# Kernel tuning notes

Hardware: AMD Instinct MI355X
Metric: run time of the kernel (lower is better)

The kernel has to match this reference:

```python
import jax, jax.numpy as jnp
import numpy as np

N_NODES = 50000
N_EDGES = 500000
HID = 128
NLAYERS = 4
NGRAPHS = 64
NODE_F = 15
EDGE_F = 3


def _init(key, shape, fan_in):
    return jax.random.normal(key, shape, dtype=jnp.float32) / np.sqrt(fan_in)


def setup_inputs() -> dict:
    key = jax.random.key(0)
    ks = jax.random.split(key, 32)
    inp = {}
    inp["x"] = jax.random.normal(ks[0], (N_NODES, NODE_F), dtype=jnp.float32)
    inp["edge_index"] = jax.random.randint(ks[1], (2, N_EDGES), 0, N_NODES, dtype=jnp.int64)
    inp["edge_attr"] = jax.random.normal(ks[2], (N_EDGES, EDGE_F), dtype=jnp.float32)
    inp["pos"] = jax.random.normal(ks[3], (N_NODES, 3), dtype=jnp.float32)
    inp["batch"] = jnp.sort(jax.random.randint(ks[4], (N_NODES,), 0, NGRAPHS, dtype=jnp.int64))
    # encoders
    inp["enc_w"] = _init(ks[5], (NODE_F, HID), NODE_F)
    inp["enc_b"] = jnp.zeros((HID,), jnp.float32)
    inp["eenc_w"] = _init(ks[6], (EDGE_F, HID), EDGE_F)
    inp["eenc_b"] = jnp.zeros((HID,), jnp.float32)
    # stacked per-layer conv params
    MIN = 2 * HID + 1  # message input dim = 257
    inp["msg_w1"] = _init(ks[7], (NLAYERS, MIN, HID), MIN)
    inp["msg_b1"] = jnp.zeros((NLAYERS, HID), jnp.float32)
    inp["msg_w2"] = _init(ks[8], (NLAYERS, HID, HID), HID)
    inp["msg_b2"] = jnp.zeros((NLAYERS, HID), jnp.float32)
    inp["upd_w1"] = _init(ks[9], (NLAYERS, 2 * HID, HID), 2 * HID)
    inp["upd_b1"] = jnp.zeros((NLAYERS, HID), jnp.float32)
    inp["upd_w2"] = _init(ks[10], (NLAYERS, HID, HID), HID)
    inp["upd_b2"] = jnp.zeros((NLAYERS, HID), jnp.float32)
    inp["ln_g"] = jnp.ones((NLAYERS, HID), jnp.float32)
    inp["ln_b"] = jnp.zeros((NLAYERS, HID), jnp.float32)
    # readout MLP (dropout is eval-mode identity)
    inp["mlp_w1"] = _init(ks[11], (HID, HID), HID)
    inp["mlp_b1"] = jnp.zeros((HID,), jnp.float32)
    inp["mlp_w2"] = _init(ks[12], (HID, HID // 2), HID)
    inp["mlp_b2"] = jnp.zeros((HID // 2,), jnp.float32)
    inp["mlp_w3"] = _init(ks[13], (HID // 2, 1), HID // 2)
    inp["mlp_b3"] = jnp.zeros((1,), jnp.float32)
    return inp


def reference(x, edge_index, edge_attr, pos, batch,
              enc_w, enc_b, eenc_w, eenc_b,
              msg_w1, msg_b1, msg_w2, msg_b2,
              upd_w1, upd_b1, upd_w2, upd_b2,
              ln_g, ln_b,
              mlp_w1, mlp_b1, mlp_w2, mlp_b2, mlp_w3, mlp_b3):
    n = x.shape[0]
    h = x @ enc_w + enc_b                      # [N, H] node encoder
    _ea = edge_attr @ eenc_w + eenc_b          # encoded but unused downstream (faithful to source)
    src = edge_index[0]                        # j (source)
    dst = edge_index[1]                        # i (target)
    dist = jnp.linalg.norm(pos[dst] - pos[src], axis=-1, keepdims=True)  # [E,1]
    for i in range(NLAYERS):
        xi = h[dst]
        xj = h[src]
        m_in = jnp.concatenate([xi, xj, dist], axis=-1)               # [E, 2H+1]
        m = jax.nn.relu(m_in @ msg_w1[i] + msg_b1[i]) @ msg_w2[i] + msg_b2[i]
        aggr = jax.ops.segment_sum(m, dst, num_segments=n)            # scatter-add -> [N,H]
        u_in = jnp.concatenate([h, aggr], axis=-1)                    # [N, 2H]
        u = jax.nn.relu(u_in @ upd_w1[i] + upd_b1[i]) @ upd_w2[i] + upd_b2[i]
        mu = jnp.mean(u, axis=-1, keepdims=True)
        var = jnp.mean((u - mu) ** 2, axis=-1, keepdims=True)
        u = (u - mu) / jnp.sqrt(var + 1e-5) * ln_g[i] + ln_b[i]
        u = jax.nn.relu(u)
        h = u if i == 0 else h + u
    # global mean pool over graphs
    cnt = jax.ops.segment_sum(jnp.ones((n, 1), h.dtype), batch, num_segments=NGRAPHS)
    pooled = jax.ops.segment_sum(h, batch, num_segments=NGRAPHS) / jnp.maximum(cnt, 1.0)
    o = jax.nn.relu(pooled @ mlp_w1 + mlp_b1)
    o = jax.nn.relu(o @ mlp_w2 + mlp_b2)
    return o @ mlp_w3 + mlp_b3                  # [NGRAPHS, 1]
```

## Files before the change

### kernel.cpp

```cpp
#include <hip/hip_runtime.h>
#include <hip/hip_bf16.h>
#include <cstdint>

#define N_NODES 50000
#define N_EDGES 500000
#define HID 128
#define NLAYERS 4
#define NGRAPHS 64
#define NTILES ((N_NODES + 63) / 64)
#define NPW 4
#define EBLOCKS ((N_NODES + NPW * 4 - 1) / (NPW * 4))

typedef float f32x4 __attribute__((ext_vector_type(4)));
typedef __bf16 bf16x8 __attribute__((ext_vector_type(8)));

__device__ float          g_h[(size_t)N_NODES * HID];
__device__ unsigned short g_hb[(size_t)N_NODES * HID];
__device__ float          g_S[(size_t)N_NODES * HID];
__device__ unsigned short g_PQ[(size_t)N_NODES * 256];
__device__ float          g_dists[N_EDGES];
__device__ int            g_srcs[N_EDGES];
__device__ int            g_cnt[N_NODES];
__device__ int            g_cursor[N_NODES];
__device__ int            g_bsum[1024];
__device__ unsigned short g_pqw[NLAYERS * 4 * 16 * 64 * 8];
__device__ float          g_wc[NLAYERS * 128 * 128];
__device__ float          g_bc[NLAYERS * 128];
__device__ unsigned short g_uw1p[NLAYERS * 8 * 8 * 64 * 8];
__device__ unsigned short g_uw2p[NLAYERS * 4 * 8 * 64 * 8];
__device__ float          g_pooled[NGRAPHS * HID];

__device__ __forceinline__ unsigned short f2bf(float f) {
    uint32_t u = __builtin_bit_cast(uint32_t, f);
    uint32_t r = (u + 0x7fffu + ((u >> 16) & 1u)) >> 16;
    return (unsigned short)r;
}
__device__ __forceinline__ float bf2f(unsigned short u) {
    return __builtin_bit_cast(float, (uint32_t)u << 16);
}

__global__ void clear_cnt_k() {
    int i = blockIdx.x * 256 + threadIdx.x;
    if (i < N_NODES) g_cnt[i] = 0;
}
__global__ void clear_pooled_k() {
    int i = blockIdx.x * 256 + threadIdx.x;
    if (i < NGRAPHS * HID) g_pooled[i] = 0.f;
}

__global__ void pack_pqw_k(const float* __restrict__ w1) {
    int lane = threadIdx.x;
    int bid = blockIdx.x;
    int nt = bid & 15, ks = (bid >> 4) & 3, L = bid >> 6;
    const float* w = w1 + (size_t)L * 257 * HID;
    int kb = ks * 32 + (lane >> 4) * 8;
    int n = nt * 16 + (lane & 15);
    unsigned short tmp[8];
#pragma unroll
    for (int j = 0; j < 8; ++j) {
        int k = kb + j;
        float v = (n < 128) ? w[(size_t)k * HID + n] : w[(size_t)(128 + k) * HID + (n - 128)];
        tmp[j] = f2bf(v);
    }
    uint4 o = make_uint4(tmp[0] | ((uint32_t)tmp[1] << 16), tmp[2] | ((uint32_t)tmp[3] << 16),
                         tmp[4] | ((uint32_t)tmp[5] << 16), tmp[6] | ((uint32_t)tmp[7] << 16));
    *(uint4*)&g_pqw[(((size_t)(L * 4 + ks) * 16 + nt) * 64 + lane) * 8] = o;
}

__global__ void wc_k(const float* __restrict__ mw2, const float* __restrict__ uw1) {
    __shared__ float row[128];
    int L = blockIdx.x >> 7, k = blockIdx.x & 127, j = threadIdx.x;
    row[j] = mw2[(size_t)L * 128 * 128 + k * 128 + j];
    __syncthreads();
    const float* u1b = uw1 + (size_t)L * 256 * 128 + 128 * 128;
    float s = 0.f;
    for (int i = 0; i < 128; ++i) s += row[i] * u1b[i * 128 + j];
    g_wc[(size_t)L * 128 * 128 + k * 128 + j] = s;
}
__global__ void bc_k(const float* __restrict__ mb2, const float* __restrict__ uw1) {
    int L = blockIdx.x, j = threadIdx.x;
    const float* u1b = uw1 + (size_t)L * 256 * 128 + 128 * 128;
    const float* b2 = mb2 + L * 128;
    float s = 0.f;
    for (int i = 0; i < 128; ++i) s += b2[i] * u1b[i * 128 + j];
    g_bc[L * 128 + j] = s;
}

__global__ void pack_u1_k(const float* __restrict__ uw1) {
    int lane = threadIdx.x;
    int bid = blockIdx.x;
    int nt = bid & 7, ks = (bid >> 3) & 7, L = bid >> 6;
    int kb = ks * 32 + (lane >> 4) * 8;
    int n = nt * 16 + (lane & 15);
    unsigned short tmp[8];
#pragma unroll
    for (int j = 0; j < 8; ++j) {
        int k = kb + j;
        float v = (k < 128) ? uw1[(size_t)L * 256 * 128 + (size_t)k * 128 + n]
                            : g_wc[(size_t)L * 128 * 128 + (size_t)(k - 128) * 128 + n];
        tmp[j] = f2bf(v);
    }
    uint4 o = make_uint4(tmp[0] | ((uint32_t)tmp[1] << 16), tmp[2] | ((uint32_t)tmp[3] << 16),
                         tmp[4] | ((uint32_t)tmp[5] << 16), tmp[6] | ((uint32_t)tmp[7] << 16));
    *(uint4*)&g_uw1p[(((size_t)(L * 8 + ks) * 8 + nt) * 64 + lane) * 8] = o;
}

__global__ void pack_w2_k(const float* __restrict__ uw2) {
    int lane = threadIdx.x;
    int bid = blockIdx.x;
    int nt = bid & 7, ks = (bid >> 3) & 3, L = bid >> 5;
    int kb = ks * 32 + (lane >> 4) * 8;
    int n = nt * 16 + (lane & 15);
    unsigned short tmp[8];
#pragma unroll
    for (int j = 0; j < 8; ++j)
        tmp[j] = f2bf(uw2[(size_t)L * 128 * 128 + (size_t)(kb + j) * 128 + n]);
    uint4 o = make_uint4(tmp[0] | ((uint32_t)tmp[1] << 16), tmp[2] | ((uint32_t)tmp[3] << 16),
                         tmp[4] | ((uint32_t)tmp[5] << 16), tmp[6] | ((uint32_t)tmp[7] << 16));
    *(uint4*)&g_uw2p[(((size_t)(L * 4 + ks) * 8 + nt) * 64 + lane) * 8] = o;
}

__global__ void encode_k(const float* __restrict__ x, const float* __restrict__ w,
                         const float* __restrict__ b) {
    __shared__ float xl[2][15];
    int t = threadIdx.x;
    int half = t >> 7;
    int node = blockIdx.x * 2 + half;
    int c = t & 127;
    if (c < 15) xl[half][c] = x[(size_t)node * 15 + c];
    __syncthreads();
    float acc = b[c];
#pragma unroll
    for (int k = 0; k < 15; ++k) acc += xl[half][k] * w[k * HID + c];
    g_h[(size_t)node * HID + c] = acc;
    g_hb[(size_t)node * HID + c] = f2bf(acc);
}

__global__ void hist_k(const int* __restrict__ ei) {
    int e = blockIdx.x * 256 + threadIdx.x;
    if (e < N_EDGES) atomicAdd(&g_cnt[ei[N_EDGES + e]], 1);
}
__global__ void scanA_k() {
    __shared__ int s[512];
    int t = threadIdx.x;
    int i = blockIdx.x * 512 + t;
    s[t] = (i < N_NODES) ? g_cnt[i] : 0;
    __syncthreads();
    for (int d = 256; d > 0; d >>= 1) {
        if (t < d) s[t] += s[t + d];
        __syncthreads();
    }
    if (t == 0) g_bsum[blockIdx.x] = s[0];
}
__global__ void scanB_k(int nb) {
    if (threadIdx.x == 0) {
        int acc = 0;
        for (int i = 0; i < nb; ++i) { int v = g_bsum[i]; g_bsum[i] = acc; acc += v; }
    }
}
__global__ void scanC_k() {
    __shared__ int s[512];
    int t = threadIdx.x;
    int i = blockIdx.x * 512 + t;
    int v = (i < N_NODES) ? g_cnt[i] : 0;
    s[t] = v;
    __syncthreads();
    for (int d = 1; d < 512; d <<= 1) {
        int add = (t >= d) ? s[t - d] : 0;
        __syncthreads();
        s[t] += add;
        __syncthreads();
    }
    if (i < N_NODES) g_cursor[i] = g_bsum[blockIdx.x] + s[t] - v;
}
__global__ void scatter_k(const int* __restrict__ ei, const float* __restrict__ pos) {
    int e = blockIdx.x * 256 + threadIdx.x;
    if (e >= N_EDGES) return;
    int s = ei[e];
    int d = ei[N_EDGES + e];
    float dx = pos[d * 3 + 0] - pos[s * 3 + 0];
    float dy = pos[d * 3 + 1] - pos[s * 3 + 1];
    float dz = pos[d * 3 + 2] - pos[s * 3 + 2];
    int p = atomicAdd(&g_cursor[d], 1);
    g_srcs[p] = s;
    g_dists[p] = sqrtf(dx * dx + dy * dy + dz * dz);
}

__global__ __launch_bounds__(256, 2)
void pq_k(int L) {
    __shared__ unsigned short Abuf[64 * 128];
    __shared__ unsigned short Obuf[64 * 264];
    const unsigned short* wp = g_pqw + (size_t)L * 4 * 16 * 64 * 8;
    int t = threadIdx.x, wave = t >> 6, lane = t & 63;
    int arow = lane & 15, kgrp = lane >> 4;
    int tile0 = blockIdx.x * 64;

    {
        int r = t >> 2, p = t & 3;
        int n = tile0 + r;
        bool valid = n < N_NODES;
#pragma unroll
        for (int q = 0; q < 4; ++q) {
            int slot = p * 4 + q;
            uint4 v = make_uint4(0, 0, 0, 0);
            if (valid) v = *(const uint4*)&g_hb[(size_t)n * HID + slot * 8];
            *(uint4*)&Abuf[r * 128 + ((slot ^ (r & 7)) << 3)] = v;
        }
    }
    __syncthreads();

    bf16x8 wv[4][4];
#pragma unroll
    for (int ks = 0; ks < 4; ++ks)
#pragma unroll
        for (int ntl = 0; ntl < 4; ++ntl)
            wv[ks][ntl] = *(const bf16x8*)&wp[((size_t)(ks * 16 + wave * 4 + ntl) * 64 + lane) * 8];

    f32x4 acc[4][4];
#pragma unroll
    for (int rf = 0; rf < 4; ++rf)
#pragma unroll
        for (int ntl = 0; ntl < 4; ++ntl) acc[rf][ntl] = (f32x4){0.f, 0.f, 0.f, 0.f};
#pragma unroll
    for (int ks = 0; ks < 4; ++ks) {
        int slot = ks * 4 + kgrp;
#pragma unroll
        for (int rf = 0; rf < 4; ++rf) {
            int row = rf * 16 + arow;
            bf16x8 a = *(const bf16x8*)&Abuf[row * 128 + ((slot ^ (row & 7)) << 3)];
#pragma unroll
            for (int ntl = 0; ntl < 4; ++ntl)
                acc[rf][ntl] = __builtin_amdgcn_mfma_f32_16x16x32_bf16(a, wv[ks][ntl], acc[rf][ntl], 0, 0, 0);
        }
    }
#pragma unroll
    for (int rf = 0; rf < 4; ++rf)
#pragma unroll
        for (int ntl = 0; ntl < 4; ++ntl) {
            int col = wave * 64 + ntl * 16 + arow;
#pragma unroll
            for (int q = 0; q < 4; ++q) {
                int row = rf * 16 + kgrp * 4 + q;
                Obuf[row * 264 + col] = f2bf(acc[rf][ntl][q]);
            }
        }
    __syncthreads();
#pragma unroll
    for (int i = 0; i < 8; ++i) {
        int k = t + i * 256;
        int row = k >> 5, cc = k & 31;
        int n = tile0 + row;
        if (n < N_NODES)
            *(uint4*)&g_PQ[(size_t)n * 256 + cc * 8] = *(const uint4*)&Obuf[row * 264 + cc * 8];
    }
}

__global__ __launch_bounds__(256, 8)
void edge_relu_k(const float* __restrict__ w1last, const float* __restrict__ b1) {
    int t = threadIdx.x, wave = t >> 6, lane = t & 63;
    int c2 = lane * 2;
    float wl0 = w1last[c2], wl1 = w1last[c2 + 1];
    float bb0 = b1[c2], bb1 = b1[c2 + 1];

    int gw = blockIdx.x * 4 + wave;
    int n0 = gw * NPW;
    int n1 = n0 + NPW < N_NODES ? n0 + NPW : N_NODES;

    for (int n = n0; n < n1; ++n) {
        int end = g_cursor[n];
        int cnt = g_cnt[n];
        int beg = end - cnt;
        uint32_t pv = *(const uint32_t*)&g_PQ[(size_t)n * 256 + c2];
        float pb0 = bf2f((unsigned short)(pv & 0xffff)) + bb0;
        float pb1 = bf2f((unsigned short)(pv >> 16)) + bb1;
        float acc0 = 0.f, acc1 = 0.f;

        for (int cb = beg; cb < end; cb += 64) {
            int mye = cb + lane;
            bool v = mye < end;
            int msrc = v ? g_srcs[mye] : 0;
            float mdist = v ? g_dists[mye] : 0.f;
            int lim = end - cb < 64 ? end - cb : 64;
            int full = lim & ~7;
            for (int b = 0; b < full; b += 8) {
                uint32_t qv[8];
#pragma unroll
                for (int j = 0; j < 8; ++j) {
                    int s = __shfl(msrc, b + j);
                    qv[j] = *(const uint32_t*)&g_PQ[(size_t)s * 256 + 128 + c2];
                }
#pragma unroll
                for (int j = 0; j < 8; ++j) {
                    float dist = __shfl(mdist, b + j);
                    acc0 += fmaxf(fmaf(dist, wl0, pb0 + bf2f((unsigned short)(qv[j] & 0xffff))), 0.f);
                    acc1 += fmaxf(fmaf(dist, wl1, pb1 + bf2f((unsigned short)(qv[j] >> 16))), 0.f);
                }
            }
            for (int j = full; j < lim; ++j) {
                int s = __shfl(msrc, j);
                float dist = __shfl(mdist, j);
                uint32_t qv = *(const uint32_t*)&g_PQ[(size_t)s * 256 + 128 + c2];
                acc0 += fmaxf(fmaf(dist, wl0, pb0 + bf2f((unsigned short)(qv & 0xffff))), 0.f);
                acc1 += fmaxf(fmaf(dist, wl1, pb1 + bf2f((unsigned short)(qv >> 16))), 0.f);
            }
        }
        *(float2*)&g_S[(size_t)n * HID + c2] = make_float2(acc0, acc1);
    }
}

__global__ __launch_bounds__(256, 4)
void upd_k(const float* __restrict__ ub1, const float* __restrict__ ub2,
           const float* __restrict__ lng, const float* __restrict__ lnb,
           int L, int first_layer, int Lpq) {
    __shared__ unsigned short Abuf[64 * 128];
    __shared__ unsigned short Hbuf[64 * 128];
    __shared__ float rsums[2][2][64];
    __shared__ float degb[64];
    const unsigned short* w1p = g_uw1p + (size_t)L * 8 * 8 * 64 * 8;
    const unsigned short* w2p = g_uw2p + (size_t)L * 4 * 8 * 64 * 8;
    int t = threadIdx.x, wave = t >> 6, lane = t & 63;
    int wr = wave >> 1, wc = wave & 1;
    int arow = lane & 15, kgrp = lane >> 4;
    int tile0 = blockIdx.x * 64;

    int sr = t >> 2, sp = t & 3;
    int sn = tile0 + sr;
    bool svalid = sn < N_NODES;

    if (sp == 0) degb[sr] = svalid ? (float)g_cnt[sn] : 0.f;
#pragma unroll
    for (int q = 0; q < 4; ++q) {
        int slot = sp * 4 + q;
        uint4 v = make_uint4(0, 0, 0, 0);
        if (svalid) v = *(const uint4*)&g_hb[(size_t)sn * HID + slot * 8];
        *(uint4*)&Abuf[sr * 128 + ((slot ^ (sr & 7)) << 3)] = v;
    }
    __syncthreads();

    f32x4 acc0[4], acc1[4];
#pragma unroll
    for (int i = 0; i < 4; ++i) { acc0[i] = (f32x4){0.f,0.f,0.f,0.f}; acc1[i] = (f32x4){0.f,0.f,0.f,0.f}; }
    int r0 = wr * 32 + arow, r1 = r0 + 16;
#pragma unroll
    for (int ks = 0; ks < 4; ++ks) {
        int slot = ks * 4 + kgrp;
        bf16x8 a0 = *(const bf16x8*)&Abuf[r0 * 128 + ((slot ^ (arow & 7)) << 3)];
        bf16x8 a1 = *(const bf16x8*)&Abuf[r1 * 128 + ((slot ^ (arow & 7)) << 3)];
#pragma unroll
        for (int ntl = 0; ntl < 4; ++ntl) {
            bf16x8 b = *(const bf16x8*)&w1p[((size_t)(ks * 8 + wc * 4 + ntl) * 64 + lane) * 8];
            acc0[ntl] = __builtin_amdgcn_mfma_f32_16x16x32_bf16(a0, b, acc0[ntl], 0, 0, 0);
            acc1[ntl] = __builtin_amdgcn_mfma_f32_16x16x32_bf16(a1, b, acc1[ntl], 0, 0, 0);
        }
    }
    __syncthreads();

#pragma unroll
    for (int q = 0; q < 4; ++q) {
        int slot = sp * 4 + q;
        uint4 v = make_uint4(0, 0, 0, 0);
        if (svalid) {
            const float* spt = &g_S[(size_t)sn * HID + slot * 8];
            float4 f0 = *(const float4*)spt;
            float4 f1 = *((const float4*)spt + 1);
            v.x = f2bf(f0.x) | ((uint32_t)f2bf(f0.y) << 16);
            v.y = f2bf(f0.z) | ((uint32_t)f2bf(f0.w) << 16);
            v.z = f2bf(f1.x) | ((uint32_t)f2bf(f1.y) << 16);
            v.w = f2bf(f1.z) | ((uint32_t)f2bf(f1.w) << 16);
        }
        *(uint4*)&Abuf[sr * 128 + ((slot ^ (sr & 7)) << 3)] = v;
    }
    __syncthreads();

#pragma unroll
    for (int ks = 0; ks < 4; ++ks) {
        int slot = ks * 4 + kgrp;
        bf16x8 a0 = *(const bf16x8*)&Abuf[r0 * 128 + ((slot ^ (arow & 7)) << 3)];
        bf16x8 a1 = *(const bf16x8*)&Abuf[r1 * 128 + ((slot ^ (arow & 7)) << 3)];
#pragma unroll
        for (int ntl = 0; ntl < 4; ++ntl) {
            bf16x8 b = *(const bf16x8*)&w1p[((size_t)((ks + 4) * 8 + wc * 4 + ntl) * 64 + lane) * 8];
            acc0[ntl] = __builtin_amdgcn_mfma_f32_16x16x32_bf16(a0, b, acc0[ntl], 0, 0, 0);
            acc1[ntl] = __builtin_amdgcn_mfma_f32_16x16x32_bf16(a1, b, acc1[ntl], 0, 0, 0);
        }
    }

    float dg0[4], dg1[4];
#pragma unroll
    for (int q = 0; q < 4; ++q) {
        dg0[q] = degb[wr * 32 + kgrp * 4 + q];
        dg1[q] = degb[wr * 32 + 16 + kgrp * 4 + q];
    }
#pragma unroll
    for (int ntl = 0; ntl < 4; ++ntl) {
        int col = wc * 64 + ntl * 16 + arow;
        float bv1 = ub1[col], bcv = g_bc[L * 128 + col];
        int slotH = col >> 3, cl = col & 7;
#pragma unroll
        for (int q = 0; q < 4; ++q) {
            int rw0 = wr * 32 + kgrp * 4 + q;
            float h0 = fmaxf(acc0[ntl][q] + dg0[q] * bcv + bv1, 0.f);
            Hbuf[rw0 * 128 + ((slotH ^ (rw0 & 7)) << 3) + cl] = f2bf(h0);
            int rw1 = rw0 + 16;
            float h1 = fmaxf(acc1[ntl][q] + dg1[q] * bcv + bv1, 0.f);
            Hbuf[rw1 * 128 + ((slotH ^ (rw1 & 7)) << 3) + cl] = f2bf(h1);
        }
    }
    __syncthreads();

    f32x4 c0[4], c1[4];
#pragma unroll
    for (int i = 0; i < 4; ++i) { c0[i] = (f32x4){0.f,0.f,0.f,0.f}; c1[i] = (f32x4){0.f,0.f,0.f,0.f}; }
#pragma unroll
    for (int ks = 0; ks < 4; ++ks) {
        int slot = ks * 4 + kgrp;
        bf16x8 a0 = *(const bf16x8*)&Hbuf[r0 * 128 + ((slot ^ (arow & 7)) << 3)];
        bf16x8 a1 = *(const bf16x8*)&Hbuf[r1 * 128 + ((slot ^ (arow & 7)) << 3)];
#pragma unroll
        for (int ntl = 0; ntl < 4; ++ntl) {
            bf16x8 b = *(const bf16x8*)&w2p[((size_t)(ks * 8 + wc * 4 + ntl) * 64 + lane) * 8];
            c0[ntl] = __builtin_amdgcn_mfma_f32_16x16x32_bf16(a0, b, c0[ntl], 0, 0, 0);
            c1[ntl] = __builtin_amdgcn_mfma_f32_16x16x32_bf16(a1, b, c1[ntl], 0, 0, 0);
        }
    }

    float bv2[4], gm[4], bt[4];
#pragma unroll
    for (int ntl = 0; ntl < 4; ++ntl) {
        int col = wc * 64 + ntl * 16 + arow;
        bv2[ntl] = ub2[col]; gm[ntl] = lng[col]; bt[ntl] = lnb[col];
    }
    float s0[4] = {0,0,0,0}, s1[4] = {0,0,0,0}, q0[4] = {0,0,0,0}, q1[4] = {0,0,0,0};
#pragma unroll
    for (int ntl = 0; ntl < 4; ++ntl)
#pragma unroll
        for (int q = 0; q < 4; ++q) {
            float v0 = c0[ntl][q] + bv2[ntl];
            float v1 = c1[ntl][q] + bv2[ntl];
            c0[ntl][q] = v0; c1[ntl][q] = v1;
            s0[q] += v0; q0[q] += v0 * v0;
            s1[q] += v1; q1[q] += v1 * v1;
        }
#pragma unroll
    for (int m = 1; m < 16; m <<= 1)
#pragma unroll
        for (int q = 0; q < 4; ++q) {
            s0[q] += __shfl_xor(s0[q], m); q0[q] += __shfl_xor(q0[q], m);
            s1[q] += __shfl_xor(s1[q], m); q1[q] += __shfl_xor(q1[q], m);
        }
    if (arow == 0) {
#pragma unroll
        for (int q = 0; q < 4; ++q) {
            int rw0 = wr * 32 + kgrp * 4 + q;
            rsums[wc][0][rw0] = s0[q]; rsums[wc][1][rw0] = q0[q];
            rsums[wc][0][rw0 + 16] = s1[q]; rsums[wc][1][rw0 + 16] = q1[q];
        }
    }
    __syncthreads();

    float mean0[4], rstd0[4], mean1[4], rstd1[4];
#pragma unroll
    for (int q = 0; q < 4; ++q) {
        int rw0 = wr * 32 + kgrp * 4 + q;
        float sm = rsums[0][0][rw0] + rsums[1][0][rw0];
        float sq = rsums[0][1][rw0] + rsums[1][1][rw0];
        mean0[q] = sm * (1.f / HID);
        rstd0[q] = rsqrtf(sq * (1.f / HID) - mean0[q] * mean0[q] + 1e-5f);
        int rw1 = rw0 + 16;
        sm = rsums[0][0][rw1] + rsums[1][0][rw1];
        sq = rsums[0][1][rw1] + rsums[1][1][rw1];
        mean1[q] = sm * (1.f / HID);
        rstd1[q] = rsqrtf(sq * (1.f / HID) - mean1[q] * mean1[q] + 1e-5f);
    }

#pragma unroll
    for (int ntl = 0; ntl < 4; ++ntl) {
        int col = wc * 64 + ntl * 16 + arow;
        int slotA = col >> 3, clA = col & 7;
#pragma unroll
        for (int q = 0; q < 4; ++q) {
            int rw0 = wr * 32 + kgrp * 4 + q;
            int row0 = tile0 + rw0;
            float u0 = fmaxf((c0[ntl][q] - mean0[q]) * rstd0[q] * gm[ntl] + bt[ntl], 0.f);
            float hr0 = (!first_layer && row0 < N_NODES) ? g_h[(size_t)row0 * HID + col] : 0.f;
            float hn0 = first_layer ? u0 : (hr0 + u0);
            c0[ntl][q] = hn0;
            Abuf[rw0 * 128 + ((slotA ^ (rw0 & 7)) << 3) + clA] = f2bf(hn0);
            int rw1 = rw0 + 16;
            int row1 = row0 + 16;
            float u1 = fmaxf((c1[ntl][q] - mean1[q]) * rstd1[q] * gm[ntl] + bt[ntl], 0.f);
            float hr1 = (!first_layer && row1 < N_NODES) ? g_h[(size_t)row1 * HID + col] : 0.f;
            float hn1 = first_layer ? u1 : (hr1 + u1);
            c1[ntl][q] = hn1;
            Abuf[rw1 * 128 + ((slotA ^ (rw1 & 7)) << 3) + clA] = f2bf(hn1);
        }
    }
    __syncthreads();

    float* FB = (float*)Hbuf;
#pragma unroll
    for (int h = 0; h < 2; ++h) {
        if (wr == h) {
#pragma unroll
            for (int ntl = 0; ntl < 4; ++ntl) {
                int col = wc * 64 + ntl * 16 + arow;
#pragma unroll
                for (int q = 0; q < 4; ++q) {
                    int lr = kgrp * 4 + q;
                    FB[lr * 128 + col] = c0[ntl][q];
                    FB[(lr + 16) * 128 + col] = c1[ntl][q];
                }
            }
        }
        __syncthreads();
#pragma unroll
        for (int i = 0; i < 4; ++i) {
            int pos = t + i * 256;
            int row = pos >> 5, cc = pos & 31;
            int n = tile0 + h * 32 + row;
            if (n < N_NODES)
                *(float4*)&g_h[(size_t)n * HID + cc * 4] = *(const float4*)&FB[row * 128 + cc * 4];
        }
        __syncthreads();
    }

    if (Lpq < 0) return;

#pragma unroll
    for (int i = 0; i < 4; ++i) {
        int pos = t + i * 256;
        int row = pos >> 4, s = pos & 15;
        int n = tile0 + row;
        if (n < N_NODES)
            *(uint4*)&g_hb[(size_t)n * HID + s * 8] =
                *(const uint4*)&Abuf[row * 128 + ((s ^ (row & 7)) << 3)];
    }

    const unsigned short* wp = g_pqw + (size_t)Lpq * 4 * 16 * 64 * 8;
#pragma unroll
    for (int h = 0; h < 2; ++h) {
        bf16x8 w3[4][2];
#pragma unroll
        for (int ks = 0; ks < 4; ++ks)
#pragma unroll
            for (int j = 0; j < 2; ++j) {
                int nt = h * 8 + wave * 2 + j;
                w3[ks][j] = *(const bf16x8*)&wp[((size_t)(ks * 16 + nt) * 64 + lane) * 8];
            }
        f32x4 a3[4][2];
#pragma unroll
        for (int rf = 0; rf < 4; ++rf)
#pragma unroll
            for (int j = 0; j < 2; ++j) a3[rf][j] = (f32x4){0.f, 0.f, 0.f, 0.f};
#pragma unroll
        for (int ks = 0; ks < 4; ++ks) {
            int slot = ks * 4 + kgrp;
#pragma unroll
            for (int rf = 0; rf < 4; ++rf) {
                int row = rf * 16 + arow;
                bf16x8 a = *(const bf16x8*)&Abuf[row * 128 + ((slot ^ (arow & 7)) << 3)];
#pragma unroll
                for (int j = 0; j < 2; ++j)
                    a3[rf][j] = __builtin_amdgcn_mfma_f32_16x16x32_bf16(a, w3[ks][j], a3[rf][j], 0, 0, 0);
            }
        }
        __syncthreads();
#pragma unroll
        for (int rf = 0; rf < 4; ++rf)
#pragma unroll
            for (int j = 0; j < 2; ++j) {
                int cl2 = (wave * 2 + j) * 16 + arow;
                int slotP = cl2 >> 3, clP = cl2 & 7;
#pragma unroll
                for (int q = 0; q < 4; ++q) {
                    int row = rf * 16 + kgrp * 4 + q;
                    Hbuf[row * 128 + ((slotP ^ (row & 7)) << 3) + clP] = f2bf(a3[rf][j][q]);
                }
            }
        __syncthreads();
#pragma unroll
        for (int i = 0; i < 4; ++i) {
            int u = t + i * 256;
            int row = u >> 4, s = u & 15;
            int n2 = tile0 + row;
            if (n2 < N_NODES)
                *(uint4*)&g_PQ[(size_t)n2 * 256 + h * 128 + s * 8] =
                    *(const uint4*)&Hbuf[row * 128 + ((s ^ (row & 7)) << 3)];
        }
    }
}

__global__ __launch_bounds__(256, 8)
void pool_k(const int* __restrict__ batch) {
    __shared__ int se[2];
    __shared__ float part[2][128];
    int b = blockIdx.x;
    int g = b >> 3, sub = b & 7;
    int t = threadIdx.x;
    if (t == 0) {
        int lo = 0, hi = N_NODES;
        while (lo < hi) { int m = (lo + hi) >> 1; if (batch[m] < g) lo = m + 1; else hi = m; }
        se[0] = lo;
        hi = N_NODES;
        while (lo < hi) { int m = (lo + hi) >> 1; if (batch[m] < g + 1) lo = m + 1; else hi = m; }
        se[1] = lo;
    }
    __syncthreads();
    int s = se[0], e = se[1];
    int c = t & 127, half = t >> 7;
    float acc = 0.f;
    for (int n = s + sub * 2 + half; n < e; n += 16) acc += g_h[(size_t)n * HID + c];
    part[half][c] = acc;
    __syncthreads();
    if (t < 128) {
        float v = part[0][t] + part[1][t];
        atomicAdd(&g_pooled[g * HID + t], v);
    }
}

__global__ void readout_k(const int* __restrict__ batch,
                          const float* __restrict__ w1, const float* __restrict__ b1,
                          const float* __restrict__ w2, const float* __restrict__ b2,
                          const float* __restrict__ w3, const float* __restrict__ b3,
                          float* __restrict__ out) {
    __shared__ float p[128], o1[128], o2[64];
    __shared__ int se[2];
    int g = blockIdx.x, t = threadIdx.x;
    if (t == 0) {
        int lo = 0, hi = N_NODES;
        while (lo < hi) { int m = (lo + hi) >> 1; if (batch[m] < g) lo = m + 1; else hi = m; }
        se[0] = lo;
        hi = N_NODES;
        while (lo < hi) { int m = (lo + hi) >> 1; if (batch[m] < g + 1) lo = m + 1; else hi = m; }
        se[1] = lo;
    }
    __syncthreads();
    float cntf = fmaxf((float)(se[1] - se[0]), 1.f);
    p[t] = g_pooled[g * HID + t] / cntf;
    __syncthreads();
    float a = b1[t];
    for (int k = 0; k < 128; ++k) a += p[k] * w1[k * 128 + t];
    o1[t] = fmaxf(a, 0.f);
    __syncthreads();
    if (t < 64) {
        float a2 = b2[t];
        for (int k = 0; k < 128; ++k) a2 += o1[k] * w2[k * 64 + t];
        o2[t] = fmaxf(a2, 0.f);
    }
    __syncthreads();
    if (t == 0) {
        float a3 = b3[0];
        for (int k = 0; k < 64; ++k) a3 += o2[k] * w3[k];
        out[g] = a3;
    }
}

extern "C" void kernel_launch(void* const* d_in, const int* in_sizes, int n_in,
                              void* d_out, int out_size, void* d_ws, size_t ws_size,
                              hipStream_t stream) {
    const float* x     = (const float*)d_in[0];
    const int*   ei    = (const int*)d_in[1];
    const float* pos   = (const float*)d_in[3];
    const int*   batch = (const int*)d_in[4];
    const float* enc_w = (const float*)d_in[5];
    const float* enc_b = (const float*)d_in[6];
    const float* msg_w1 = (const float*)d_in[9];
    const float* msg_b1 = (const float*)d_in[10];
    const float* msg_w2 = (const float*)d_in[11];
    const float* msg_b2 = (const float*)d_in[12];
    const float* upd_w1 = (const float*)d_in[13];
    const float* upd_b1 = (const float*)d_in[14];
    const float* upd_w2 = (const float*)d_in[15];
    const float* upd_b2 = (const float*)d_in[16];
    const float* ln_g   = (const float*)d_in[17];
    const float* ln_b   = (const float*)d_in[18];
    const float* mw1 = (const float*)d_in[19];
    const float* mb1 = (const float*)d_in[20];
    const float* mw2 = (const float*)d_in[21];
    const float* mb2 = (const float*)d_in[22];
    const float* mw3 = (const float*)d_in[23];
    const float* mb3 = (const float*)d_in[24];
    float* out = (float*)d_out;
    (void)d_ws; (void)ws_size; (void)in_sizes; (void)n_in; (void)out_size;

    pack_pqw_k<<<NLAYERS * 4 * 16, 64, 0, stream>>>(msg_w1);
    wc_k<<<NLAYERS * 128, 128, 0, stream>>>(msg_w2, upd_w1);
    bc_k<<<NLAYERS, 128, 0, stream>>>(msg_b2, upd_w1);
    pack_u1_k<<<NLAYERS * 8 * 8, 64, 0, stream>>>(upd_w1);
    pack_w2_k<<<NLAYERS * 4 * 8, 64, 0, stream>>>(upd_w2);

    encode_k<<<N_NODES / 2, 256, 0, stream>>>(x, enc_w, enc_b);

    clear_cnt_k<<<(N_NODES + 255) / 256, 256, 0, stream>>>();
    hist_k<<<(N_EDGES + 255) / 256, 256, 0, stream>>>(ei);
    int nb = (N_NODES + 511) / 512;
    scanA_k<<<nb, 512, 0, stream>>>();
    scanB_k<<<1, 64, 0, stream>>>(nb);
    scanC_k<<<nb, 512, 0, stream>>>();
    scatter_k<<<(N_EDGES + 255) / 256, 256, 0, stream>>>(ei, pos);

    pq_k<<<NTILES, 256, 0, stream>>>(0);
    clear_pooled_k<<<32, 256, 0, stream>>>();
    for (int L = 0; L < NLAYERS; ++L) {
        edge_relu_k<<<EBLOCKS, 256, 0, stream>>>(
            msg_w1 + (size_t)L * 257 * HID + 256 * HID, msg_b1 + L * HID);
        upd_k<<<NTILES, 256, 0, stream>>>(
            upd_b1 + L * HID, upd_b2 + L * HID, ln_g + L * HID, ln_b + L * HID,
            L, L == 0 ? 1 : 0, L < NLAYERS - 1 ? L + 1 : -1);
    }

    pool_k<<<NGRAPHS * 8, 256, 0, stream>>>(batch);
    readout_k<<<NGRAPHS, 128, 0, stream>>>(batch, mw1, mb1, mw2, mb2, mw3, mb3, out);
}
```

Baseline: 561.9 us.

## Shrink update-kernel tiles to 32 rows and pack edge src/dist into int2

The update kernel now processes 32-node tiles instead of 64, with each of the four waves owning a 32-column slice and all 32 rows. This halves shared memory per block, raises the occupancy hint from 4 to 6, and launches twice as many blocks. Separately, the CSR edge arrays (source index and distance) are merged into one int2 array so the edge kernel fetches both with a single load. Smaller tiles reload the weights more often per node, and the LayerNorm reduction now sums four partials instead of two.

```diff
diff --git a/kernel.cpp b/kernel.cpp
--- a/kernel.cpp
+++ b/kernel.cpp
@@ -8,6 +8,7 @@
 #define NLAYERS 4
 #define NGRAPHS 64
 #define NTILES ((N_NODES + 63) / 64)
+#define NT32 ((N_NODES + 31) / 32)
 #define NPW 4
 #define EBLOCKS ((N_NODES + NPW * 4 - 1) / (NPW * 4))
 
@@ -18,8 +19,7 @@
 __device__ unsigned short g_hb[(size_t)N_NODES * HID];
 __device__ float          g_S[(size_t)N_NODES * HID];
 __device__ unsigned short g_PQ[(size_t)N_NODES * 256];
-__device__ float          g_dists[N_EDGES];
-__device__ int            g_srcs[N_EDGES];
+__device__ int2           g_edge[N_EDGES];
 __device__ int            g_cnt[N_NODES];
 __device__ int            g_cursor[N_NODES];
 __device__ int            g_bsum[1024];
@@ -181,9 +181,9 @@
     float dx = pos[d * 3 + 0] - pos[s * 3 + 0];
     float dy = pos[d * 3 + 1] - pos[s * 3 + 1];
     float dz = pos[d * 3 + 2] - pos[s * 3 + 2];
+    float dist = sqrtf(dx * dx + dy * dy + dz * dz);
     int p = atomicAdd(&g_cursor[d], 1);
-    g_srcs[p] = s;
-    g_dists[p] = sqrtf(dx * dx + dy * dy + dz * dz);
+    g_edge[p] = make_int2(s, __builtin_bit_cast(int, dist));
 }
 
 __global__ __launch_bounds__(256, 2)
@@ -278,8 +278,9 @@
         for (int cb = beg; cb < end; cb += 64) {
             int mye = cb + lane;
             bool v = mye < end;
-            int msrc = v ? g_srcs[mye] : 0;
-            float mdist = v ? g_dists[mye] : 0.f;
+            int2 ed = v ? g_edge[mye] : make_int2(0, 0);
+            int msrc = ed.x;
+            float mdist = __builtin_bit_cast(float, ed.y);
             int lim = end - cb < 64 ? end - cb : 64;
             int full = lim & ~7;
             for (int b = 0; b < full; b += 8) {
@@ -308,47 +309,46 @@
     }
 }
 
-__global__ __launch_bounds__(256, 4)
+__global__ __launch_bounds__(256, 6)
 void upd_k(const float* __restrict__ ub1, const float* __restrict__ ub2,
            const float* __restrict__ lng, const float* __restrict__ lnb,
            int L, int first_layer, int Lpq) {
-    __shared__ unsigned short Abuf[64 * 128];
-    __shared__ unsigned short Hbuf[64 * 128];
-    __shared__ float rsums[2][2][64];
-    __shared__ float degb[64];
+    __shared__ unsigned short Abuf[32 * 128];
+    __shared__ unsigned short Hbuf[32 * 128];
+    __shared__ float rsums[4][2][32];
+    __shared__ float degb[32];
     const unsigned short* w1p = g_uw1p + (size_t)L * 8 * 8 * 64 * 8;
     const unsigned short* w2p = g_uw2p + (size_t)L * 4 * 8 * 64 * 8;
     int t = threadIdx.x, wave = t >> 6, lane = t & 63;
-    int wr = wave >> 1, wc = wave & 1;
     int arow = lane & 15, kgrp = lane >> 4;
-    int tile0 = blockIdx.x * 64;
-
-    int sr = t >> 2, sp = t & 3;
+    int tile0 = blockIdx.x * 32;
+
+    int sr = t >> 3, sp = t & 7;
     int sn = tile0 + sr;
     bool svalid = sn < N_NODES;
 
     if (sp == 0) degb[sr] = svalid ? (float)g_cnt[sn] : 0.f;
 #pragma unroll
-    for (int q = 0; q < 4; ++q) {
-        int slot = sp * 4 + q;
+    for (int q = 0; q < 2; ++q) {
+        int slot = sp * 2 + q;
         uint4 v = make_uint4(0, 0, 0, 0);
         if (svalid) v = *(const uint4*)&g_hb[(size_t)sn * HID + slot * 8];
         *(uint4*)&Abuf[sr * 128 + ((slot ^ (sr & 7)) << 3)] = v;
     }
     __syncthreads();
 
-    f32x4 acc0[4], acc1[4];
-#pragma unroll
-    for (int i = 0; i < 4; ++i) { acc0[i] = (f32x4){0.f,0.f,0.f,0.f}; acc1[i] = (f32x4){0.f,0.f,0.f,0.f}; }
-    int r0 = wr * 32 + arow, r1 = r0 + 16;
+    f32x4 acc0[2], acc1[2];
+#pragma unroll
+    for (int i = 0; i < 2; ++i) { acc0[i] = (f32x4){0.f,0.f,0.f,0.f}; acc1[i] = (f32x4){0.f,0.f,0.f,0.f}; }
+    int r0 = arow, r1 = arow + 16;
 #pragma unroll
     for (int ks = 0; ks < 4; ++ks) {
         int slot = ks * 4 + kgrp;
         bf16x8 a0 = *(const bf16x8*)&Abuf[r0 * 128 + ((slot ^ (arow & 7)) << 3)];
         bf16x8 a1 = *(const bf16x8*)&Abuf[r1 * 128 + ((slot ^ (arow & 7)) << 3)];
 #pragma unroll
-        for (int ntl = 0; ntl < 4; ++ntl) {
-            bf16x8 b = *(const bf16x8*)&w1p[((size_t)(ks * 8 + wc * 4 + ntl) * 64 + lane) * 8];
+        for (int ntl = 0; ntl < 2; ++ntl) {
+            bf16x8 b = *(const bf16x8*)&w1p[((size_t)(ks * 8 + wave * 2 + ntl) * 64 + lane) * 8];
             acc0[ntl] = __builtin_amdgcn_mfma_f32_16x16x32_bf16(a0, b, acc0[ntl], 0, 0, 0);
             acc1[ntl] = __builtin_amdgcn_mfma_f32_16x16x32_bf16(a1, b, acc1[ntl], 0, 0, 0);
         }
@@ -356,8 +356,8 @@
     __syncthreads();
 
 #pragma unroll
-    for (int q = 0; q < 4; ++q) {
-        int slot = sp * 4 + q;
+    for (int q = 0; q < 2; ++q) {
+        int slot = sp * 2 + q;
         uint4 v = make_uint4(0, 0, 0, 0);
         if (svalid) {
             const float* spt = &g_S[(size_t)sn * HID + slot * 8];
@@ -378,8 +378,8 @@
         bf16x8 a0 = *(const bf16x8*)&Abuf[r0 * 128 + ((slot ^ (arow & 7)) << 3)];
         bf16x8 a1 = *(const bf16x8*)&Abuf[r1 * 128 + ((slot ^ (arow & 7)) << 3)];
 #pragma unroll
-        for (int ntl = 0; ntl < 4; ++ntl) {
-            bf16x8 b = *(const bf16x8*)&w1p[((size_t)((ks + 4) * 8 + wc * 4 + ntl) * 64 + lane) * 8];
+        for (int ntl = 0; ntl < 2; ++ntl) {
+            bf16x8 b = *(const bf16x8*)&w1p[((size_t)((ks + 4) * 8 + wave * 2 + ntl) * 64 + lane) * 8];
             acc0[ntl] = __builtin_amdgcn_mfma_f32_16x16x32_bf16(a0, b, acc0[ntl], 0, 0, 0);
             acc1[ntl] = __builtin_amdgcn_mfma_f32_16x16x32_bf16(a1, b, acc1[ntl], 0, 0, 0);
         }
@@ -388,17 +388,17 @@
     float dg0[4], dg1[4];
 #pragma unroll
     for (int q = 0; q < 4; ++q) {
-        dg0[q] = degb[wr * 32 + kgrp * 4 + q];
-        dg1[q] = degb[wr * 32 + 16 + kgrp * 4 + q];
-    }
-#pragma unroll
-    for (int ntl = 0; ntl < 4; ++ntl) {
-        int col = wc * 64 + ntl * 16 + arow;
+        dg0[q] = degb[kgrp * 4 + q];
+        dg1[q] = degb[16 + kgrp * 4 + q];
+    }
+#pragma unroll
+    for (int ntl = 0; ntl < 2; ++ntl) {
+        int col = wave * 32 + ntl * 16 + arow;
         float bv1 = ub1[col], bcv = g_bc[L * 128 + col];
         int slotH = col >> 3, cl = col & 7;
 #pragma unroll
         for (int q = 0; q < 4; ++q) {
-            int rw0 = wr * 32 + kgrp * 4 + q;
+            int rw0 = kgrp * 4 + q;
             float h0 = fmaxf(acc0[ntl][q] + dg0[q] * bcv + bv1, 0.f);
             Hbuf[rw0 * 128 + ((slotH ^ (rw0 & 7)) << 3) + cl] = f2bf(h0);
             int rw1 = rw0 + 16;
@@ -408,31 +408,31 @@
     }
     __syncthreads();
 
-    f32x4 c0[4], c1[4];
-#pragma unroll
-    for (int i = 0; i < 4; ++i) { c0[i] = (f32x4){0.f,0.f,0.f,0.f}; c1[i] = (f32x4){0.f,0.f,0.f,0.f}; }
+    f32x4 c0[2], c1[2];
+#pragma unroll
+    for (int i = 0; i < 2; ++i) { c0[i] = (f32x4){0.f,0.f,0.f,0.f}; c1[i] = (f32x4){0.f,0.f,0.f,0.f}; }
 #pragma unroll
     for (int ks = 0; ks < 4; ++ks) {
         int slot = ks * 4 + kgrp;
         bf16x8 a0 = *(const bf16x8*)&Hbuf[r0 * 128 + ((slot ^ (arow & 7)) << 3)];
         bf16x8 a1 = *(const bf16x8*)&Hbuf[r1 * 128 + ((slot ^ (arow & 7)) << 3)];
 #pragma unroll
-        for (int ntl = 0; ntl < 4; ++ntl) {
-            bf16x8 b = *(const bf16x8*)&w2p[((size_t)(ks * 8 + wc * 4 + ntl) * 64 + lane) * 8];
+        for (int ntl = 0; ntl < 2; ++ntl) {
+            bf16x8 b = *(const bf16x8*)&w2p[((size_t)(ks * 8 + wave * 2 + ntl) * 64 + lane) * 8];
             c0[ntl] = __builtin_amdgcn_mfma_f32_16x16x32_bf16(a0, b, c0[ntl], 0, 0, 0);
             c1[ntl] = __builtin_amdgcn_mfma_f32_16x16x32_bf16(a1, b, c1[ntl], 0, 0, 0);
         }
     }
 
-    float bv2[4], gm[4], bt[4];
-#pragma unroll
-    for (int ntl = 0; ntl < 4; ++ntl) {
-        int col = wc * 64 + ntl * 16 + arow;
+    float bv2[2], gm[2], bt[2];
+#pragma unroll
+    for (int ntl = 0; ntl < 2; ++ntl) {
+        int col = wave * 32 + ntl * 16 + arow;
         bv2[ntl] = ub2[col]; gm[ntl] = lng[col]; bt[ntl] = lnb[col];
     }
     float s0[4] = {0,0,0,0}, s1[4] = {0,0,0,0}, q0[4] = {0,0,0,0}, q1[4] = {0,0,0,0};
 #pragma unroll
-    for (int ntl = 0; ntl < 4; ++ntl)
+    for (int ntl = 0; ntl < 2; ++ntl)
 #pragma unroll
         for (int q = 0; q < 4; ++q) {
             float v0 = c0[ntl][q] + bv2[ntl];
@@ -451,9 +451,9 @@
     if (arow == 0) {
 #pragma unroll
         for (int q = 0; q < 4; ++q) {
-            int rw0 = wr * 32 + kgrp * 4 + q;
-            rsums[wc][0][rw0] = s0[q]; rsums[wc][1][rw0] = q0[q];
-            rsums[wc][0][rw0 + 16] = s1[q]; rsums[wc][1][rw0 + 16] = q1[q];
+            int rw0 = kgrp * 4 + q;
+            rsums[wave][0][rw0] = s0[q]; rsums[wave][1][rw0] = q0[q];
+            rsums[wave][0][rw0 + 16] = s1[q]; rsums[wave][1][rw0 + 16] = q1[q];
         }
     }
     __syncthreads();
@@ -461,25 +461,25 @@
     float mean0[4], rstd0[4], mean1[4], rstd1[4];
 #pragma unroll
     for (int q = 0; q < 4; ++q) {
-        int rw0 = wr * 32 + kgrp * 4 + q;
-        float sm = rsums[0][0][rw0] + rsums[1][0][rw0];
-        float sq = rsums[0][1][rw0] + rsums[1][1][rw0];
+        int rw0 = kgrp * 4 + q;
+        float sm = rsums[0][0][rw0] + rsums[1][0][rw0] + rsums[2][0][rw0] + rsums[3][0][rw0];
+        float sq = rsums[0][1][rw0] + rsums[1][1][rw0] + rsums[2][1][rw0] + rsums[3][1][rw0];
         mean0[q] = sm * (1.f / HID);
         rstd0[q] = rsqrtf(sq * (1.f / HID) - mean0[q] * mean0[q] + 1e-5f);
         int rw1 = rw0 + 16;
-        sm = rsums[0][0][rw1] + rsums[1][0][rw1];
-        sq = rsums[0][1][rw1] + rsums[1][1][rw1];
+        sm = rsums[0][0][rw1] + rsums[1][0][rw1] + rsums[2][0][rw1] + rsums[3][0][rw1];
+        sq = rsums[0][1][rw1] + rsums[1][1][rw1] + rsums[2][1][rw1] + rsums[3][1][rw1];
         mean1[q] = sm * (1.f / HID);
         rstd1[q] = rsqrtf(sq * (1.f / HID) - mean1[q] * mean1[q] + 1e-5f);
     }
 
 #pragma unroll
-    for (int ntl = 0; ntl < 4; ++ntl) {
-        int col = wc * 64 + ntl * 16 + arow;
+    for (int ntl = 0; ntl < 2; ++ntl) {
+        int col = wave * 32 + ntl * 16 + arow;
         int slotA = col >> 3, clA = col & 7;
 #pragma unroll
         for (int q = 0; q < 4; ++q) {
-            int rw0 = wr * 32 + kgrp * 4 + q;
+            int rw0 = kgrp * 4 + q;
             int row0 = tile0 + rw0;
             float u0 = fmaxf((c0[ntl][q] - mean0[q]) * rstd0[q] * gm[ntl] + bt[ntl], 0.f);
             float hr0 = (!first_layer && row0 < N_NODES) ? g_h[(size_t)row0 * HID + col] : 0.f;
@@ -498,36 +498,45 @@
     __syncthreads();
 
     float* FB = (float*)Hbuf;
-#pragma unroll
-    for (int h = 0; h < 2; ++h) {
-        if (wr == h) {
-#pragma unroll
-            for (int ntl = 0; ntl < 4; ++ntl) {
-                int col = wc * 64 + ntl * 16 + arow;
-#pragma unroll
-                for (int q = 0; q < 4; ++q) {
-                    int lr = kgrp * 4 + q;
-                    FB[lr * 128 + col] = c0[ntl][q];
-                    FB[(lr + 16) * 128 + col] = c1[ntl][q];
-                }
-            }
-        }
-        __syncthreads();
-#pragma unroll
-        for (int i = 0; i < 4; ++i) {
+    {
+#pragma unroll
+        for (int ntl = 0; ntl < 2; ++ntl) {
+            int col = wave * 32 + ntl * 16 + arow;
+#pragma unroll
+            for (int q = 0; q < 4; ++q) FB[(kgrp * 4 + q) * 128 + col] = c0[ntl][q];
+        }
+        __syncthreads();
+#pragma unroll
+        for (int i = 0; i < 2; ++i) {
             int pos = t + i * 256;
             int row = pos >> 5, cc = pos & 31;
-            int n = tile0 + h * 32 + row;
+            int n = tile0 + row;
             if (n < N_NODES)
                 *(float4*)&g_h[(size_t)n * HID + cc * 4] = *(const float4*)&FB[row * 128 + cc * 4];
         }
         __syncthreads();
+#pragma unroll
+        for (int ntl = 0; ntl < 2; ++ntl) {
+            int col = wave * 32 + ntl * 16 + arow;
+#pragma unroll
+            for (int q = 0; q < 4; ++q) FB[(kgrp * 4 + q) * 128 + col] = c1[ntl][q];
+        }
+        __syncthreads();
+#pragma unroll
+        for (int i = 0; i < 2; ++i) {
+            int pos = t + i * 256;
+            int row = pos >> 5, cc = pos & 31;
+            int n = tile0 + 16 + row;
+            if (n < N_NODES)
+                *(float4*)&g_h[(size_t)n * HID + cc * 4] = *(const float4*)&FB[row * 128 + cc * 4];
+        }
+        __syncthreads();
     }
 
     if (Lpq < 0) return;
 
 #pragma unroll
-    for (int i = 0; i < 4; ++i) {
+    for (int i = 0; i < 2; ++i) {
         int pos = t + i * 256;
         int row = pos >> 4, s = pos & 15;
         int n = tile0 + row;
@@ -547,39 +556,38 @@
                 int nt = h * 8 + wave * 2 + j;
                 w3[ks][j] = *(const bf16x8*)&wp[((size_t)(ks * 16 + nt) * 64 + lane) * 8];
             }
-        f32x4 a3[4][2];
-#pragma unroll
-        for (int rf = 0; rf < 4; ++rf)
+        f32x4 a3[2][2];
+#pragma unroll
+        for (int rf = 0; rf < 2; ++rf)
 #pragma unroll
             for (int j = 0; j < 2; ++j) a3[rf][j] = (f32x4){0.f, 0.f, 0.f, 0.f};
 #pragma unroll
         for (int ks = 0; ks < 4; ++ks) {
             int slot = ks * 4 + kgrp;
-#pragma unroll
-            for (int rf = 0; rf < 4; ++rf) {
-                int row = rf * 16 + arow;
-                bf16x8 a = *(const bf16x8*)&Abuf[row * 128 + ((slot ^ (arow & 7)) << 3)];
-#pragma unroll
-                for (int j = 0; j < 2; ++j)
-                    a3[rf][j] = __builtin_amdgcn_mfma_f32_16x16x32_bf16(a, w3[ks][j], a3[rf][j], 0, 0, 0);
+            bf16x8 a0 = *(const bf16x8*)&Abuf[r0 * 128 + ((slot ^ (arow & 7)) << 3)];
+            bf16x8 a1 = *(const bf16x8*)&Abuf[r1 * 128 + ((slot ^ (arow & 7)) << 3)];
+#pragma unroll
+            for (int j = 0; j < 2; ++j) {
+                a3[0][j] = __builtin_amdgcn_mfma_f32_16x16x32_bf16(a0, w3[ks][j], a3[0][j], 0, 0, 0);
+                a3[1][j] = __builtin_amdgcn_mfma_f32_16x16x32_bf16(a1, w3[ks][j], a3[1][j], 0, 0, 0);
             }
         }
         __syncthreads();
 #pragma unroll
-        for (int rf = 0; rf < 4; ++rf)
-#pragma unroll
-            for (int j = 0; j < 2; ++j) {
-                int cl2 = (wave * 2 + j) * 16 + arow;
-                int slotP = cl2 >> 3, clP = cl2 & 7;
-#pragma unroll
-                for (int q = 0; q < 4; ++q) {
-                    int row = rf * 16 + kgrp * 4 + q;
-                    Hbuf[row * 128 + ((slotP ^ (row & 7)) << 3) + clP] = f2bf(a3[rf][j][q]);
-                }
+        for (int j = 0; j < 2; ++j) {
+            int cl2 = (wave * 2 + j) * 16 + arow;
+            int slotP = cl2 >> 3, clP = cl2 & 7;
+#pragma unroll
+            for (int q = 0; q < 4; ++q) {
+                int row = kgrp * 4 + q;
+                Hbuf[row * 128 + ((slotP ^ (row & 7)) << 3) + clP] = f2bf(a3[0][j][q]);
+                int row2 = row + 16;
+                Hbuf[row2 * 128 + ((slotP ^ (row2 & 7)) << 3) + clP] = f2bf(a3[1][j][q]);
             }
-        __syncthreads();
-#pragma unroll
-        for (int i = 0; i < 4; ++i) {
+        }
+        __syncthreads();
+#pragma unroll
+        for (int i = 0; i < 2; ++i) {
             int u = t + i * 256;
             int row = u >> 4, s = u & 15;
             int n2 = tile0 + row;
@@ -587,6 +595,7 @@
                 *(uint4*)&g_PQ[(size_t)n2 * 256 + h * 128 + s * 8] =
                     *(const uint4*)&Hbuf[row * 128 + ((s ^ (row & 7)) << 3)];
         }
+        __syncthreads();
     }
 }
 
@@ -704,7 +713,7 @@
     for (int L = 0; L < NLAYERS; ++L) {
         edge_relu_k<<<EBLOCKS, 256, 0, stream>>>(
             msg_w1 + (size_t)L * 257 * HID + 256 * HID, msg_b1 + L * HID);
-        upd_k<<<NTILES, 256, 0, stream>>>(
+        upd_k<<<NT32, 256, 0, stream>>>(
             upd_b1 + L * HID, upd_b2 + L * HID, ln_g + L * HID, ln_b + L * HID,
             L, L == 0 ? 1 : 0, L < NLAYERS - 1 ? L + 1 : -1);
     }
```

Result: slower. 748.6 us (+33.2%).
